# Kernel optimization log

Measured on AMD Instinct MI355X. Metric: run time of the kernel, lower is better.

Reference implementation:

```python
import jax, jax.numpy as jnp
import numpy as np

HEADS = 8
DIM_HEAD = 64
DIM = 512
EPS = 1e-5


def setup_inputs() -> dict:
    key = jax.random.key(0)
    ks = jax.random.split(key, 4)
    b, n = 4, 2048
    inner = HEADS * DIM_HEAD
    x = jax.random.normal(ks[0], (b, n, DIM), dtype=jnp.float32)
    pose_bias = jax.random.normal(ks[1], (b, n), dtype=jnp.float32)
    ln_gamma = jnp.ones((DIM,), dtype=jnp.float32)
    ln_beta = jnp.zeros((DIM,), dtype=jnp.float32)
    w_qkv = jax.random.normal(ks[2], (DIM, 3 * inner), dtype=jnp.float32) * (DIM ** -0.5)
    w_out = jax.random.normal(ks[3], (inner, DIM), dtype=jnp.float32) * (inner ** -0.5)
    beta = jnp.float32(0.5)
    return {"x": x, "pose_bias": pose_bias, "ln_gamma": ln_gamma,
            "ln_beta": ln_beta, "w_qkv": w_qkv, "w_out": w_out, "beta": beta}


def reference(x, pose_bias, ln_gamma, ln_beta, w_qkv, w_out, beta):
    b, n, d = x.shape
    h, dh = HEADS, DIM_HEAD
    scale = dh ** -0.5
    # LayerNorm (biased variance, eps=1e-5, affine)
    mu = jnp.mean(x, axis=-1, keepdims=True)
    var = jnp.mean(jnp.square(x - mu), axis=-1, keepdims=True)
    xn = (x - mu) * jax.lax.rsqrt(var + EPS) * ln_gamma + ln_beta
    # fused QKV projection (no bias)
    qkv = xn @ w_qkv                                  # [b, n, 3*h*dh]
    q, k, v = jnp.split(qkv, 3, axis=-1)
    def to_heads(t):
        return t.reshape(b, n, h, dh).transpose(0, 2, 1, 3)  # [b, h, n, dh]
    q, k, v = to_heads(q), to_heads(k), to_heads(v)
    dots = jnp.einsum('bhnd,bhmd->bhnm', q, k) * scale  # [b, h, n, n]
    # additive pose bias: beta * (bias_i + bias_j), broadcast over heads
    pose_attn = beta * (pose_bias[:, None, :, None] + pose_bias[:, None, None, :])
    dots = dots + pose_attn
    attn = jax.nn.softmax(dots, axis=-1)
    out = jnp.einsum('bhnm,bhmd->bhnd', attn, v)       # [b, h, n, dh]
    out = out.transpose(0, 2, 1, 3).reshape(b, n, h * dh)
    return out @ w_out
```

## Files before the change

kernel.cpp:

```cpp
#include <hip/hip_runtime.h>
#include <hip/hip_bf16.h>

#define NH    8
#define DH    64
#define DIMD  512
#define NCTX  2048
#define NB    4
#define NROWS (NB * NCTX)
#define QKVN  (3 * DIMD)

typedef __attribute__((ext_vector_type(8))) short bf16x8;
typedef __attribute__((ext_vector_type(4))) float f32x4;

#define INV_LN2 1.44269504f
#define SCLOG   (0.125f * INV_LN2)

__device__ __forceinline__ unsigned short f2bits(float f) {
  unsigned u = __float_as_uint(f);
  u += 0x7fffu + ((u >> 16) & 1u);
  return (unsigned short)(u >> 16);
}
__device__ __forceinline__ float bits2f(unsigned short u) {
  return __uint_as_float(((unsigned)u) << 16);
}
__device__ __forceinline__ unsigned pk2(float lo, float hi) {
  __hip_bfloat162 h = __float22bfloat162_rn(float2{lo, hi});
  union { __hip_bfloat162 h; unsigned u; } c; c.h = h; return c.u;
}

__device__ __forceinline__ void gll16(const void* g, void* l) {
  __builtin_amdgcn_global_load_lds(
      (const __attribute__((address_space(1))) unsigned int*)g,
      (__attribute__((address_space(3))) unsigned int*)l, 16, 0, 0);
}
__device__ __forceinline__ void gll4(const void* g, void* l) {
  __builtin_amdgcn_global_load_lds(
      (const __attribute__((address_space(1))) unsigned int*)g,
      (__attribute__((address_space(3))) unsigned int*)l, 4, 0, 0);
}

__global__ __launch_bounds__(256) void lntc_kernel(
    const float* __restrict__ x,
    const float* __restrict__ gamma,
    const float* __restrict__ beta,
    unsigned short* __restrict__ xn,
    const float* __restrict__ in0, unsigned short* __restrict__ out0,
    const float* __restrict__ in1, unsigned short* __restrict__ out1,
    const float* __restrict__ pb, const float* __restrict__ betap,
    float* __restrict__ pbl) {
  __shared__ float T[64][65];
  if (blockIdx.x < 2048) {
    const int wid  = threadIdx.x >> 6;
    const int lane = threadIdx.x & 63;
    const int row  = blockIdx.x * 4 + wid;
    const float* xr = x + (size_t)row * DIMD + lane * 8;
    float v[8];
    const float4 a = *reinterpret_cast<const float4*>(xr);
    const float4 b = *reinterpret_cast<const float4*>(xr + 4);
    v[0] = a.x; v[1] = a.y; v[2] = a.z; v[3] = a.w;
    v[4] = b.x; v[5] = b.y; v[6] = b.z; v[7] = b.w;
    float s = 0.f;
#pragma unroll
    for (int i = 0; i < 8; ++i) s += v[i];
#pragma unroll
    for (int off = 32; off; off >>= 1) s += __shfl_down(s, off);
    s = __shfl(s, 0);
    const float mu = s * (1.f / DIMD);
    float ss = 0.f;
#pragma unroll
    for (int i = 0; i < 8; ++i) { float d = v[i] - mu; ss += d * d; }
#pragma unroll
    for (int off = 32; off; off >>= 1) ss += __shfl_down(ss, off);
    ss = __shfl(ss, 0);
    const float inv = rsqrtf(ss * (1.f / DIMD) + 1e-5f);
    const float4 g0 = *reinterpret_cast<const float4*>(gamma + lane * 8);
    const float4 g1 = *reinterpret_cast<const float4*>(gamma + lane * 8 + 4);
    const float4 b0 = *reinterpret_cast<const float4*>(beta + lane * 8);
    const float4 b1 = *reinterpret_cast<const float4*>(beta + lane * 8 + 4);
    float g[8] = {g0.x, g0.y, g0.z, g0.w, g1.x, g1.y, g1.z, g1.w};
    float be[8] = {b0.x, b0.y, b0.z, b0.w, b1.x, b1.y, b1.z, b1.w};
    bf16x8 o;
#pragma unroll
    for (int i = 0; i < 8; ++i)
      o[i] = (short)f2bits((v[i] - mu) * inv * g[i] + be[i]);
    *reinterpret_cast<bf16x8*>(xn + (size_t)row * DIMD + lane * 8) = o;
  } else if (blockIdx.x < 2432) {
    const int t = blockIdx.x - 2048;
    const int bx = t % 24, rest = t / 24;
    const int by = rest % 8, z = rest / 8;
    const int C = z ? DIMD : QKVN;
    if (z && bx >= DIMD / 64) return;
    const float* in = z ? in1 : in0;
    unsigned short* out = z ? out1 : out0;
    const int r0 = by * 64, c0 = bx * 64;
    const int ty = threadIdx.x >> 4, tx = threadIdx.x & 15;
#pragma unroll
    for (int i = 0; i < 4; ++i) {
      const int r = ty + i * 16;
      const float4 v = *reinterpret_cast<const float4*>(
          in + (size_t)(r0 + r) * C + c0 + tx * 4);
      T[r][tx * 4 + 0] = v.x; T[r][tx * 4 + 1] = v.y;
      T[r][tx * 4 + 2] = v.z; T[r][tx * 4 + 3] = v.w;
    }
    __syncthreads();
#pragma unroll
    for (int i = 0; i < 4; ++i) {
      const int c = ty + i * 16;
      ushort4 o;
      o.x = f2bits(T[tx * 4 + 0][c]); o.y = f2bits(T[tx * 4 + 1][c]);
      o.z = f2bits(T[tx * 4 + 2][c]); o.w = f2bits(T[tx * 4 + 3][c]);
      *reinterpret_cast<ushort4*>(out + (size_t)(c0 + c) * DIMD + r0 + tx * 4) = o;
    }
  } else {
    const int t2 = blockIdx.x - 2432;
    const float bl2 = betap[0] * INV_LN2;
    const int idx = t2 * 2048 + threadIdx.x * 8;
    const float4 a = *reinterpret_cast<const float4*>(pb + idx);
    const float4 b = *reinterpret_cast<const float4*>(pb + idx + 4);
    float4 oa = {bl2 * a.x, bl2 * a.y, bl2 * a.z, bl2 * a.w};
    float4 ob = {bl2 * b.x, bl2 * b.y, bl2 * b.z, bl2 * b.w};
    *reinterpret_cast<float4*>(pbl + idx) = oa;
    *reinterpret_cast<float4*>(pbl + idx + 4) = ob;
  }
}

__device__ __forceinline__ void storeC(float* C, size_t idx, float v) { C[idx] = v; }
__device__ __forceinline__ void storeC(unsigned short* C, size_t idx, float v) { C[idx] = f2bits(v); }

template <typename CT, bool QS>
__global__ __launch_bounds__(256) void ggemm_kernel(
    const unsigned short* __restrict__ A, const unsigned short* __restrict__ Bt,
    CT* __restrict__ C, unsigned short* __restrict__ vtg, int M, int N, int K) {
  __shared__ __align__(16) unsigned short As[128 * 64];
  __shared__ __align__(16) unsigned short Bs[128 * 64];
  const int tid  = threadIdx.x;
  const int wave = tid >> 6, lane = tid & 63;
  const int quad = lane >> 4, l16 = lane & 15;
  const int wr = wave >> 1, wc = wave & 1;
  const int nwg  = gridDim.x * gridDim.y;
  const int orig = blockIdx.y * gridDim.x + blockIdx.x;
  const int swz  = (orig & 7) * (nwg >> 3) + (orig >> 3);
  const int tm0 = (swz / gridDim.x) * 128, tn0 = (swz % gridDim.x) * 128;
  const bool vswap = QS && (tn0 >= 2 * DIMD);
  const int srow = wave * 8 + (lane >> 3);
  const int ssh  = (((lane & 7) * 16) ^ ((lane >> 3) << 4)) >> 1;
  const unsigned short* ap = A + (size_t)(tm0 + srow) * K + ssh;
  const unsigned short* bp = Bt + (size_t)(tn0 + srow) * K + ssh;
  const int xs = (l16 & 7) << 3;
  f32x4 acc[4][4];
#pragma unroll
  for (int i = 0; i < 4; ++i)
#pragma unroll
    for (int j = 0; j < 4; ++j) acc[i][j] = (f32x4){0.f, 0.f, 0.f, 0.f};

  for (int k0 = 0; k0 < K; k0 += 64) {
#pragma unroll
    for (int i = 0; i < 4; ++i) {
      gll16(ap + (size_t)(i * 32) * K + k0, &As[i * 2048 + wave * 512]);
      gll16(bp + (size_t)(i * 32) * K + k0, &Bs[i * 2048 + wave * 512]);
    }
    __syncthreads();
#pragma unroll
    for (int kc = 0; kc < 2; ++kc) {
      const int kk = ((kc * 32 + quad * 8) ^ xs);
      bf16x8 af[4], bfr[4];
#pragma unroll
      for (int i = 0; i < 4; ++i)
        af[i] = *reinterpret_cast<const bf16x8*>(&As[(wr * 64 + i * 16 + l16) * 64 + kk]);
#pragma unroll
      for (int j = 0; j < 4; ++j)
        bfr[j] = *reinterpret_cast<const bf16x8*>(&Bs[(wc * 64 + j * 16 + l16) * 64 + kk]);
      if (vswap) {
#pragma unroll
        for (int i = 0; i < 4; ++i)
#pragma unroll
          for (int j = 0; j < 4; ++j)
            acc[i][j] = __builtin_amdgcn_mfma_f32_16x16x32_bf16(bfr[j], af[i], acc[i][j], 0, 0, 0);
      } else {
#pragma unroll
        for (int i = 0; i < 4; ++i)
#pragma unroll
          for (int j = 0; j < 4; ++j)
            acc[i][j] = __builtin_amdgcn_mfma_f32_16x16x32_bf16(af[i], bfr[j], acc[i][j], 0, 0, 0);
      }
    }
    __syncthreads();
  }
  if (vswap) {
#pragma unroll
    for (int j = 0; j < 4; ++j)
#pragma unroll
      for (int i = 0; i < 4; ++i)
#pragma unroll
        for (int r = 0; r < 4; ++r) {
          const int vcol = tn0 - 2 * DIMD + wc * 64 + j * 16 + quad * 4 + r;
          const int hi = vcol >> 6, d = vcol & 63;
          const int rowc = tm0 + wr * 64 + i * 16 + l16;
          const int bi = rowc >> 11, jc = rowc & (NCTX - 1);
          vtg[((size_t)(bi * NH + hi) * DH + d) * NCTX + jc] = f2bits(acc[i][j][r]);
        }
  } else {
#pragma unroll
    for (int j = 0; j < 4; ++j) {
      const int col = tn0 + wc * 64 + j * 16 + l16;
      const float scl = (QS && col < DIMD) ? SCLOG : 1.0f;
#pragma unroll
      for (int i = 0; i < 4; ++i)
#pragma unroll
        for (int r = 0; r < 4; ++r)
          storeC(C, (size_t)(tm0 + wr * 64 + i * 16 + quad * 4 + r) * N + col,
                 acc[i][j][r] * scl);
    }
  }
}

template <typename CT, bool QS>
__global__ __launch_bounds__(256) void mgemm_kernel(
    const unsigned short* __restrict__ A, const unsigned short* __restrict__ Bt,
    CT* __restrict__ C, int M, int N, int K) {
  __shared__ __align__(16) unsigned short As[128][72];
  __shared__ __align__(16) unsigned short Bs[128][72];
  const int tid  = threadIdx.x;
  const int wave = tid >> 6, lane = tid & 63;
  const int quad = lane >> 4, l16 = lane & 15;
  const int wr = wave >> 1, wc = wave & 1;
  const int nwg  = gridDim.x * gridDim.y;
  const int orig = blockIdx.y * gridDim.x + blockIdx.x;
  const int swz  = (orig & 7) * (nwg >> 3) + (orig >> 3);
  const int tm0 = (swz / gridDim.x) * 128, tn0 = (swz % gridDim.x) * 128;
  const int srow = tid >> 3;
  const int schunk = (tid & 7) * 8;
  f32x4 acc[4][4];
#pragma unroll
  for (int i = 0; i < 4; ++i)
#pragma unroll
    for (int j = 0; j < 4; ++j) acc[i][j] = (f32x4){0.f, 0.f, 0.f, 0.f};

  bf16x8 ra[4], rb[4];
#pragma unroll
  for (int p = 0; p < 4; ++p) {
    const int r = srow + p * 32;
    ra[p] = *reinterpret_cast<const bf16x8*>(A + (size_t)(tm0 + r) * K + schunk);
    rb[p] = *reinterpret_cast<const bf16x8*>(Bt + (size_t)(tn0 + r) * K + schunk);
  }
  for (int k0 = 0; k0 < K; k0 += 64) {
#pragma unroll
    for (int p = 0; p < 4; ++p) {
      const int r = srow + p * 32;
      *reinterpret_cast<bf16x8*>(&As[r][schunk]) = ra[p];
      *reinterpret_cast<bf16x8*>(&Bs[r][schunk]) = rb[p];
    }
    __syncthreads();
    if (k0 + 64 < K) {
#pragma unroll
      for (int p = 0; p < 4; ++p) {
        const int r = srow + p * 32;
        ra[p] = *reinterpret_cast<const bf16x8*>(A + (size_t)(tm0 + r) * K + k0 + 64 + schunk);
        rb[p] = *reinterpret_cast<const bf16x8*>(Bt + (size_t)(tn0 + r) * K + k0 + 64 + schunk);
      }
    }
#pragma unroll
    for (int kc = 0; kc < 2; ++kc) {
      const int kk = kc * 32 + quad * 8;
      bf16x8 af[4], bfr[4];
#pragma unroll
      for (int i = 0; i < 4; ++i)
        af[i] = *reinterpret_cast<const bf16x8*>(&As[wr * 64 + i * 16 + l16][kk]);
#pragma unroll
      for (int j = 0; j < 4; ++j)
        bfr[j] = *reinterpret_cast<const bf16x8*>(&Bs[wc * 64 + j * 16 + l16][kk]);
#pragma unroll
      for (int i = 0; i < 4; ++i)
#pragma unroll
        for (int j = 0; j < 4; ++j)
          acc[i][j] = __builtin_amdgcn_mfma_f32_16x16x32_bf16(af[i], bfr[j], acc[i][j], 0, 0, 0);
    }
    __syncthreads();
  }
#pragma unroll
  for (int j = 0; j < 4; ++j) {
    const int col = tn0 + wc * 64 + j * 16 + l16;
    const float scl = (QS && col < DIMD) ? SCLOG : 1.0f;
#pragma unroll
    for (int i = 0; i < 4; ++i)
#pragma unroll
      for (int r = 0; r < 4; ++r)
        storeC(C, (size_t)(tm0 + wr * 64 + i * 16 + quad * 4 + r) * N + col,
               acc[i][j][r] * scl);
  }
}

__global__ __launch_bounds__(512, 4) void fattn_kernel(
    const unsigned short* __restrict__ qkv,
    const unsigned short* __restrict__ vtg,
    const float* __restrict__ pbl,
    unsigned short* __restrict__ out) {
  __shared__ __align__(16) unsigned short lds[2][8320];

  const int qt = blockIdx.x, hi = blockIdx.y, bi = blockIdx.z;
  const int tid  = threadIdx.x;
  const int wave = tid >> 6, lane = tid & 63;
  const int quad = lane >> 4, l16 = lane & 15;
  const int wq = wave & 3, wk = wave >> 2;
  const int qrow0 = qt * 128;
  const unsigned short* base  = qkv + (size_t)bi * NCTX * QKVN + hi * DH;
  const unsigned short* vbase = vtg + (size_t)(bi * NH + hi) * DH * NCTX;
  const float* pbase = pbl + (size_t)bi * NCTX;

  const int sr8 = lane >> 3;
  const int ssh = ((((lane & 7) * 16) ^ (sr8 << 4)) >> 1);
  const unsigned short* kp0 = base + (size_t)(wave * 8 + sr8) * QKVN + DIMD + ssh;
  const unsigned short* vp0 = vbase + (size_t)(wave * 8 + sr8) * NCTX + ssh;
  const float* pp = pbase + lane;

#define STAGE(buf)                                    \
  gll16(kp0, &(buf)[wave * 512]);                     \
  gll16(vp0, &(buf)[4096 + wave * 512]);              \
  if (tid < 64) gll4(pp, &(buf)[8192]);               \
  kp0 += (size_t)64 * QKVN; vp0 += 64; pp += 64;

  bf16x8 qf[2][2];
#pragma unroll
  for (int u = 0; u < 2; ++u)
#pragma unroll
    for (int h = 0; h < 2; ++h)
      qf[u][h] = *reinterpret_cast<const bf16x8*>(
          base + (size_t)(qrow0 + wq * 32 + u * 16 + l16) * QKVN + h * 32 + quad * 8);

  const int xs = (l16 & 7) << 3;
  const int kofs0 = (wk * 32 + l16) * 64 + ((quad * 8) ^ xs);
  const int kofs1 = (wk * 32 + l16) * 64 + ((32 + quad * 8) ^ xs);
  const int vofs  = 4096 + l16 * 64 + ((wk * 32 + quad * 8) ^ xs);
  const int pofs  = wk * 32 + quad * 4;

  const bf16x8 ones = {16256, 16256, 16256, 16256, 16256, 16256, 16256, 16256};

  STAGE(lds[0]);
  __syncthreads();

  f32x4 O[2][4], accl[2];
#pragma unroll
  for (int u = 0; u < 2; ++u) {
    accl[u] = (f32x4){0.f, 0.f, 0.f, 0.f};
#pragma unroll
    for (int s = 0; s < 4; ++s) O[u][s] = (f32x4){0.f, 0.f, 0.f, 0.f};
  }

  for (int kt = 0; kt < 32; ++kt) {
    const unsigned short* bc = lds[kt & 1];
    if (kt < 31) { STAGE(lds[(kt & 1) ^ 1]); }
    const float* pblf = (const float*)(bc + 8192);
    f32x4 sfr[2][2];
#pragma unroll
    for (int t = 0; t < 2; ++t) {
      const bf16x8 kf0 = *reinterpret_cast<const bf16x8*>(&bc[kofs0 + t * 1024]);
      const bf16x8 kf1 = *reinterpret_cast<const bf16x8*>(&bc[kofs1 + t * 1024]);
      const f32x4 bias = *reinterpret_cast<const f32x4*>(&pblf[pofs + t * 16]);
#pragma unroll
      for (int u = 0; u < 2; ++u) {
        f32x4 acc = bias;
        acc = __builtin_amdgcn_mfma_f32_16x16x32_bf16(kf0, qf[u][0], acc, 0, 0, 0);
        acc = __builtin_amdgcn_mfma_f32_16x16x32_bf16(kf1, qf[u][1], acc, 0, 0, 0);
        sfr[t][u] = acc;
      }
    }
    bf16x8 pf[2];
#pragma unroll
    for (int u = 0; u < 2; ++u) {
      unsigned x0 = pk2(__builtin_amdgcn_exp2f(sfr[0][u][0]),
                        __builtin_amdgcn_exp2f(sfr[0][u][1]));
      unsigned x1 = pk2(__builtin_amdgcn_exp2f(sfr[0][u][2]),
                        __builtin_amdgcn_exp2f(sfr[0][u][3]));
      unsigned y0 = pk2(__builtin_amdgcn_exp2f(sfr[1][u][0]),
                        __builtin_amdgcn_exp2f(sfr[1][u][1]));
      unsigned y1 = pk2(__builtin_amdgcn_exp2f(sfr[1][u][2]),
                        __builtin_amdgcn_exp2f(sfr[1][u][3]));
      asm("v_permlane32_swap_b32 %0, %1" : "+v"(x0), "+v"(y0));
      asm("v_permlane32_swap_b32 %0, %1" : "+v"(x1), "+v"(y1));
      asm("v_permlane16_swap_b32 %0, %1" : "+v"(x0), "+v"(y0));
      asm("v_permlane16_swap_b32 %0, %1" : "+v"(x1), "+v"(y1));
      union { unsigned q[4]; bf16x8 v; } pu;
      pu.q[0] = x0; pu.q[1] = x1; pu.q[2] = y0; pu.q[3] = y1;
      pf[u] = pu.v;
    }
    {
      accl[0] = __builtin_amdgcn_mfma_f32_16x16x32_bf16(pf[0], ones, accl[0], 0, 0, 0);
      accl[1] = __builtin_amdgcn_mfma_f32_16x16x32_bf16(pf[1], ones, accl[1], 0, 0, 0);
#pragma unroll
      for (int s = 0; s < 4; ++s) {
        const bf16x8 bv = *reinterpret_cast<const bf16x8*>(&bc[vofs + s * 1024]);
        O[0][s] = __builtin_amdgcn_mfma_f32_16x16x32_bf16(pf[0], bv, O[0][s], 0, 0, 0);
        O[1][s] = __builtin_amdgcn_mfma_f32_16x16x32_bf16(pf[1], bv, O[1][s], 0, 0, 0);
      }
    }
    __syncthreads();
  }
#undef STAGE
  unsigned short* Ob = (unsigned short*)lds;
  float* lb = (float*)((unsigned short*)lds + 8704);
  if (wk == 1) {
#pragma unroll
    for (int u = 0; u < 2; ++u) {
#pragma unroll
      for (int s = 0; s < 4; ++s)
#pragma unroll
        for (int r = 0; r < 4; ++r)
          Ob[(wq * 32 + u * 16 + quad * 4 + r) * 68 + s * 16 + l16] = f2bits(O[u][s][r]);
      if (l16 == 0)
#pragma unroll
        for (int r = 0; r < 4; ++r)
          lb[128 + wq * 32 + u * 16 + quad * 4 + r] = accl[u][r];
    }
  } else {
#pragma unroll
    for (int u = 0; u < 2; ++u)
      if (l16 == 0)
#pragma unroll
        for (int r = 0; r < 4; ++r)
          lb[wq * 32 + u * 16 + quad * 4 + r] = accl[u][r];
  }
  __syncthreads();
  if (wk == 0) {
#pragma unroll
    for (int u = 0; u < 2; ++u)
#pragma unroll
      for (int r = 0; r < 4; ++r) {
        const int ql = wq * 32 + u * 16 + quad * 4 + r;
        const float linv = 1.f / (lb[ql] + lb[128 + ql]);
        const size_t orow = ((size_t)bi * NCTX + qrow0 + ql) * DIMD + hi * DH;
#pragma unroll
        for (int s = 0; s < 4; ++s)
          out[orow + s * 16 + l16] =
              f2bits((O[u][s][r] + bits2f(Ob[ql * 68 + s * 16 + l16])) * linv);
      }
  }
}

extern "C" void kernel_launch(void* const* d_in, const int* in_sizes, int n_in,
                              void* d_out, int out_size, void* d_ws, size_t ws_size,
                              hipStream_t stream) {
  const float* x     = (const float*)d_in[0];
  const float* pose  = (const float*)d_in[1];
  const float* gam   = (const float*)d_in[2];
  const float* bet   = (const float*)d_in[3];
  const float* wqkv  = (const float*)d_in[4];
  const float* wout  = (const float*)d_in[5];
  const float* betap = (const float*)d_in[6];
  float* out = (float*)d_out;

  unsigned short* xn    = (unsigned short*)d_ws;
  unsigned short* qkvb  = xn + (size_t)NROWS * DIMD;
  unsigned short* wqkvT = qkvb + (size_t)NROWS * QKVN;
  unsigned short* woutT = wqkvT + (size_t)QKVN * DIMD;
  unsigned short* vtg   = woutT + (size_t)DIMD * DIMD;
  float*          pbl   = (float*)(vtg + (size_t)NB * NH * DH * NCTX);
  unsigned short* aout  = xn;

  lntc_kernel<<<2048 + 384 + 4, 256, 0, stream>>>(
      x, gam, bet, xn, wqkv, wqkvT, wout, woutT, pose, betap, pbl);
  ggemm_kernel<unsigned short, true><<<dim3(QKVN / 128, NROWS / 128), 256, 0, stream>>>(
      xn, wqkvT, qkvb, vtg, NROWS, QKVN, DIMD);
  fattn_kernel<<<dim3(NCTX / 128, NH, NB), 512, 0, stream>>>(qkvb, vtg, pbl, aout);
  mgemm_kernel<float, false><<<dim3(DIMD / 128, NROWS / 128), 256, 0, stream>>>(
      aout, woutT, out, NROWS, DIMD, DIMD);
}
```

Before: 159.3 us.

## Double key tile per iteration to halve barrier and loop overhead

Each main-loop iteration of the attention kernel now stages and processes 128 keys instead of 64. The K, V and bias staging layouts, swizzles and LDS offsets are reworked to match, and the loop count drops from 32 to 16. This halves the number of __syncthreads and staging rounds and gives the scheduler more independent MFMA work per iteration. The cost is doubled LDS use per block (about 66KB), which may limit occupancy against the launch bound of 4 blocks.

```diff
diff --git a/kernel.cpp b/kernel.cpp
--- a/kernel.cpp
+++ b/kernel.cpp
@@ -295,7 +295,7 @@
     const unsigned short* __restrict__ vtg,
     const float* __restrict__ pbl,
     unsigned short* __restrict__ out) {
-  __shared__ __align__(16) unsigned short lds[2][8320];
+  __shared__ __align__(16) unsigned short lds[2][16640];
 
   const int qt = blockIdx.x, hi = blockIdx.y, bi = blockIdx.z;
   const int tid  = threadIdx.x;
@@ -310,14 +310,21 @@
   const int sr8 = lane >> 3;
   const int ssh = ((((lane & 7) * 16) ^ (sr8 << 4)) >> 1);
   const unsigned short* kp0 = base + (size_t)(wave * 8 + sr8) * QKVN + DIMD + ssh;
-  const unsigned short* vp0 = vbase + (size_t)(wave * 8 + sr8) * NCTX + ssh;
-  const float* pp = pbase + lane;
-
-#define STAGE(buf)                                    \
-  gll16(kp0, &(buf)[wave * 512]);                     \
-  gll16(vp0, &(buf)[4096 + wave * 512]);              \
-  if (tid < 64) gll4(pp, &(buf)[8192]);               \
-  kp0 += (size_t)64 * QKVN; vp0 += 64; pp += 64;
+  const unsigned short* kp1 = kp0 + (size_t)64 * QKVN;
+  const int vd  = wave * 4 + (lane >> 4);
+  const int vsh = ((lane & 15) * 8) ^ ((vd & 7) << 3);
+  const unsigned short* vp0 = vbase + (size_t)vd * NCTX + vsh;
+  const unsigned short* vp1 = vp0 + (size_t)32 * NCTX;
+  const float* pp = pbase + tid;
+
+#define STAGE(buf)                                      \
+  gll16(kp0, &(buf)[wave * 512]);                       \
+  gll16(kp1, &(buf)[4096 + wave * 512]);                \
+  gll16(vp0, &(buf)[8192 + wave * 512]);                \
+  gll16(vp1, &(buf)[12288 + wave * 512]);               \
+  if (tid < 128) gll4(pp, &(buf)[16384 + wave * 128]);  \
+  kp0 += (size_t)128 * QKVN; kp1 += (size_t)128 * QKVN; \
+  vp0 += 128; vp1 += 128; pp += 128;
 
   bf16x8 qf[2][2];
 #pragma unroll
@@ -328,10 +335,11 @@
           base + (size_t)(qrow0 + wq * 32 + u * 16 + l16) * QKVN + h * 32 + quad * 8);
 
   const int xs = (l16 & 7) << 3;
-  const int kofs0 = (wk * 32 + l16) * 64 + ((quad * 8) ^ xs);
-  const int kofs1 = (wk * 32 + l16) * 64 + ((32 + quad * 8) ^ xs);
-  const int vofs  = 4096 + l16 * 64 + ((wk * 32 + quad * 8) ^ xs);
-  const int pofs  = wk * 32 + quad * 4;
+  const int kofs0 = (wk * 64 + l16) * 64 + ((quad * 8) ^ xs);
+  const int kofs1 = (wk * 64 + l16) * 64 + ((32 + quad * 8) ^ xs);
+  const int vofsA = 8192 + l16 * 128 + ((wk * 64 + quad * 8) ^ xs);
+  const int vofsB = 8192 + l16 * 128 + ((wk * 64 + 32 + quad * 8) ^ xs);
+  const int pofs  = wk * 64 + quad * 4;
 
   const bf16x8 ones = {16256, 16256, 16256, 16256, 16256, 16256, 16256, 16256};
 
@@ -346,51 +354,60 @@
     for (int s = 0; s < 4; ++s) O[u][s] = (f32x4){0.f, 0.f, 0.f, 0.f};
   }
 
-  for (int kt = 0; kt < 32; ++kt) {
+  for (int kt = 0; kt < 16; ++kt) {
     const unsigned short* bc = lds[kt & 1];
-    if (kt < 31) { STAGE(lds[(kt & 1) ^ 1]); }
-    const float* pblf = (const float*)(bc + 8192);
-    f32x4 sfr[2][2];
-#pragma unroll
-    for (int t = 0; t < 2; ++t) {
-      const bf16x8 kf0 = *reinterpret_cast<const bf16x8*>(&bc[kofs0 + t * 1024]);
-      const bf16x8 kf1 = *reinterpret_cast<const bf16x8*>(&bc[kofs1 + t * 1024]);
-      const f32x4 bias = *reinterpret_cast<const f32x4*>(&pblf[pofs + t * 16]);
+    if (kt < 15) { STAGE(lds[(kt & 1) ^ 1]); }
+    const float* pblf = (const float*)(bc + 16384);
+    bf16x8 pfA[2], pfB[2];
+#pragma unroll
+    for (int b = 0; b < 2; ++b) {
+      f32x4 sfr[2][2];
+#pragma unroll
+      for (int tt = 0; tt < 2; ++tt) {
+        const int t = b * 2 + tt;
+        const bf16x8 kf0 = *reinterpret_cast<const bf16x8*>(&bc[kofs0 + t * 1024]);
+        const bf16x8 kf1 = *reinterpret_cast<const bf16x8*>(&bc[kofs1 + t * 1024]);
+        const f32x4 bias = *reinterpret_cast<const f32x4*>(&pblf[pofs + t * 16]);
+#pragma unroll
+        for (int u = 0; u < 2; ++u) {
+          f32x4 acc = bias;
+          acc = __builtin_amdgcn_mfma_f32_16x16x32_bf16(kf0, qf[u][0], acc, 0, 0, 0);
+          acc = __builtin_amdgcn_mfma_f32_16x16x32_bf16(kf1, qf[u][1], acc, 0, 0, 0);
+          sfr[tt][u] = acc;
+        }
+      }
 #pragma unroll
       for (int u = 0; u < 2; ++u) {
-        f32x4 acc = bias;
-        acc = __builtin_amdgcn_mfma_f32_16x16x32_bf16(kf0, qf[u][0], acc, 0, 0, 0);
-        acc = __builtin_amdgcn_mfma_f32_16x16x32_bf16(kf1, qf[u][1], acc, 0, 0, 0);
-        sfr[t][u] = acc;
-      }
-    }
-    bf16x8 pf[2];
-#pragma unroll
-    for (int u = 0; u < 2; ++u) {
-      unsigned x0 = pk2(__builtin_amdgcn_exp2f(sfr[0][u][0]),
-                        __builtin_amdgcn_exp2f(sfr[0][u][1]));
-      unsigned x1 = pk2(__builtin_amdgcn_exp2f(sfr[0][u][2]),
-                        __builtin_amdgcn_exp2f(sfr[0][u][3]));
-      unsigned y0 = pk2(__builtin_amdgcn_exp2f(sfr[1][u][0]),
-                        __builtin_amdgcn_exp2f(sfr[1][u][1]));
-      unsigned y1 = pk2(__builtin_amdgcn_exp2f(sfr[1][u][2]),
-                        __builtin_amdgcn_exp2f(sfr[1][u][3]));
-      asm("v_permlane32_swap_b32 %0, %1" : "+v"(x0), "+v"(y0));
-      asm("v_permlane32_swap_b32 %0, %1" : "+v"(x1), "+v"(y1));
-      asm("v_permlane16_swap_b32 %0, %1" : "+v"(x0), "+v"(y0));
-      asm("v_permlane16_swap_b32 %0, %1" : "+v"(x1), "+v"(y1));
-      union { unsigned q[4]; bf16x8 v; } pu;
-      pu.q[0] = x0; pu.q[1] = x1; pu.q[2] = y0; pu.q[3] = y1;
-      pf[u] = pu.v;
+        unsigned x0 = pk2(__builtin_amdgcn_exp2f(sfr[0][u][0]),
+                          __builtin_amdgcn_exp2f(sfr[0][u][1]));
+        unsigned x1 = pk2(__builtin_amdgcn_exp2f(sfr[0][u][2]),
+                          __builtin_amdgcn_exp2f(sfr[0][u][3]));
+        unsigned y0 = pk2(__builtin_amdgcn_exp2f(sfr[1][u][0]),
+                          __builtin_amdgcn_exp2f(sfr[1][u][1]));
+        unsigned y1 = pk2(__builtin_amdgcn_exp2f(sfr[1][u][2]),
+                          __builtin_amdgcn_exp2f(sfr[1][u][3]));
+        asm("v_permlane32_swap_b32 %0, %1" : "+v"(x0), "+v"(y0));
+        asm("v_permlane32_swap_b32 %0, %1" : "+v"(x1), "+v"(y1));
+        asm("v_permlane16_swap_b32 %0, %1" : "+v"(x0), "+v"(y0));
+        asm("v_permlane16_swap_b32 %0, %1" : "+v"(x1), "+v"(y1));
+        union { unsigned q[4]; bf16x8 v; } pu;
+        pu.q[0] = x0; pu.q[1] = x1; pu.q[2] = y0; pu.q[3] = y1;
+        if (b == 0) pfA[u] = pu.v; else pfB[u] = pu.v;
+      }
     }
     {
-      accl[0] = __builtin_amdgcn_mfma_f32_16x16x32_bf16(pf[0], ones, accl[0], 0, 0, 0);
-      accl[1] = __builtin_amdgcn_mfma_f32_16x16x32_bf16(pf[1], ones, accl[1], 0, 0, 0);
+      accl[0] = __builtin_amdgcn_mfma_f32_16x16x32_bf16(pfA[0], ones, accl[0], 0, 0, 0);
+      accl[1] = __builtin_amdgcn_mfma_f32_16x16x32_bf16(pfA[1], ones, accl[1], 0, 0, 0);
+      accl[0] = __builtin_amdgcn_mfma_f32_16x16x32_bf16(pfB[0], ones, accl[0], 0, 0, 0);
+      accl[1] = __builtin_amdgcn_mfma_f32_16x16x32_bf16(pfB[1], ones, accl[1], 0, 0, 0);
 #pragma unroll
       for (int s = 0; s < 4; ++s) {
-        const bf16x8 bv = *reinterpret_cast<const bf16x8*>(&bc[vofs + s * 1024]);
-        O[0][s] = __builtin_amdgcn_mfma_f32_16x16x32_bf16(pf[0], bv, O[0][s], 0, 0, 0);
-        O[1][s] = __builtin_amdgcn_mfma_f32_16x16x32_bf16(pf[1], bv, O[1][s], 0, 0, 0);
+        const bf16x8 bvA = *reinterpret_cast<const bf16x8*>(&bc[vofsA + s * 2048]);
+        const bf16x8 bvB = *reinterpret_cast<const bf16x8*>(&bc[vofsB + s * 2048]);
+        O[0][s] = __builtin_amdgcn_mfma_f32_16x16x32_bf16(pfA[0], bvA, O[0][s], 0, 0, 0);
+        O[1][s] = __builtin_amdgcn_mfma_f32_16x16x32_bf16(pfA[1], bvA, O[1][s], 0, 0, 0);
+        O[0][s] = __builtin_amdgcn_mfma_f32_16x16x32_bf16(pfB[0], bvB, O[0][s], 0, 0, 0);
+        O[1][s] = __builtin_amdgcn_mfma_f32_16x16x32_bf16(pfB[1], bvB, O[1][s], 0, 0, 0);
       }
     }
     __syncthreads();
```

Result: no change. 159.8 us (+0.3%).
